# Optimization experiments

Hardware: AMD Instinct MI355X
Metric: run time of the kernel (lower is better)

Reference implementation:

```python
import jax, jax.numpy as jnp
import numpy as np

_SAMPLING_EPS = 1e-5


def setup_inputs() -> dict:
    key = jax.random.key(0)
    k1, k2, k3, k4, k5 = jax.random.split(key, 5)
    B, V = 128, 128000
    logits = jax.random.normal(k1, (B, V), dtype=jnp.float32)
    temperature = jax.random.uniform(k2, (B,), dtype=jnp.float32)  # some rows < eps -> greedy
    top_k = jax.random.randint(k3, (B,), 1, 64, dtype=jnp.int32)   # in [1, 63]
    top_p = jax.random.uniform(k4, (B,), dtype=jnp.float32, minval=0.05, maxval=1.0)
    noise_u = jax.random.uniform(k5, (B, V), dtype=jnp.float32, minval=1e-10, maxval=1.0)
    return {"logits": logits, "temperature": temperature, "top_k": top_k,
            "top_p": top_p, "noise_u": noise_u, "max_num_logprobs": 5}


def _apply_top_k_top_p(logits, k, p):
    # Faithful to vLLM: ascending sort, top-k threshold mask, top-p cumsum mask, scatter back.
    B, V = logits.shape
    order = jnp.argsort(logits, axis=-1)                       # ascending, [B, V]
    logits_sort = jnp.take_along_axis(logits, order, axis=-1)
    neg_inf = jnp.float32(-jnp.inf)
    # top-k: pivot value at position V - k; everything strictly below it -> -inf
    pivot_idx = (V - k.astype(jnp.int32))[:, None]             # [B, 1]
    pivot = jnp.take_along_axis(logits_sort, pivot_idx, axis=-1)
    logits_sort = jnp.where(logits_sort < pivot, neg_inf, logits_sort)
    # top-p: softmax over sorted logits, cumsum, drop prefix with mass <= 1 - p (keep last)
    probs_sort = jax.nn.softmax(logits_sort, axis=-1)
    probs_sum = jnp.cumsum(probs_sort, axis=-1)
    top_p_mask = probs_sum <= (1.0 - p)[:, None]
    top_p_mask = top_p_mask.at[:, -1].set(False)
    logits_sort = jnp.where(top_p_mask, neg_inf, logits_sort)
    # scatter back to original vocab order
    rows = jnp.arange(B)[:, None]
    return jnp.zeros_like(logits).at[rows, order].set(logits_sort)


def reference(logits, temperature, top_k, top_p, noise_u, max_num_logprobs):
    # temperature scaling (temp < eps means greedy; divide by 1.0 instead)
    temp = jnp.where(temperature < _SAMPLING_EPS, 1.0, temperature)
    logits = logits.astype(jnp.float32) / temp[:, None]
    # top-k / top-p filtering
    logits = _apply_top_k_top_p(logits, top_k, top_p)
    # probabilities and sampling
    probs = jax.nn.softmax(logits, axis=-1)
    greedy = jnp.argmax(probs, axis=-1)
    q = -jnp.log(noise_u)                                      # Exp(1) noise (q.exponential_())
    random = jnp.argmax(probs / q, axis=-1)
    sampled = jnp.where(temperature < _SAMPLING_EPS, greedy, random).astype(jnp.int32)
    # top-k logprobs
    logprobs = jax.nn.log_softmax(logits, axis=-1)
    topk_logprobs, topk_indices = jax.lax.top_k(logprobs, max_num_logprobs)
    return sampled, topk_indices.astype(jnp.int32), topk_logprobs
```

## Files before the change

### kernel.cpp

```cpp
#include <hip/hip_runtime.h>
#include <math.h>
#include <stdint.h>

#define BT     256
#define NCHUNK 8
#define CAP    4096
#define TOPC   64
#define TILE   (BT * 8)
#define NC     (NCHUNK * TOPC)

__device__ __forceinline__ unsigned f2ord(float f) {
    unsigned u = __float_as_uint(f);
    return u ^ ((u & 0x80000000u) ? 0xFFFFFFFFu : 0x80000000u);
}
__device__ __forceinline__ float ord2f(unsigned k) {
    unsigned u = (k & 0x80000000u) ? (k ^ 0x80000000u) : (k ^ 0xFFFFFFFFu);
    return __uint_as_float(u);
}

__device__ unsigned radix_select_compact(unsigned* s_key, int* s_idx,
                                         unsigned* s_ckey, int* s_cidx,
                                         unsigned* s_hist, unsigned* p_cnt2,
                                         unsigned n, int tid)
{
    unsigned prefix = 0u;
    int remaining = TOPC;
    for (int shift = 28; shift >= 0; shift -= 4) {
        if (tid < 16) s_hist[tid] = 0u;
        __syncthreads();
        for (unsigned i = (unsigned)tid; i < n; i += BT) {
            unsigned k = s_key[i];
            bool ing = (shift == 28) || ((k >> (shift + 4)) == (prefix >> (shift + 4)));
            if (ing) atomicAdd(&s_hist[(k >> shift) & 15u], 1u);
        }
        __syncthreads();
        int cum = 0; int b = 0;
        for (int bb = 15; bb >= 0; --bb) {
            cum += (int)s_hist[bb];
            if (cum >= remaining) { b = bb; break; }
        }
        remaining -= (cum - (int)s_hist[b]);
        prefix |= ((unsigned)b) << shift;
        __syncthreads();
    }
    if (tid == 0) *p_cnt2 = 0u;
    __syncthreads();
    for (unsigned i = (unsigned)tid; i < n; i += BT) {
        unsigned k = s_key[i];
        if (k > prefix) {
            unsigned pos = atomicAdd(p_cnt2, 1u);
            s_ckey[pos] = k; s_cidx[pos] = s_idx[i];
        }
    }
    __syncthreads();
    for (unsigned i = (unsigned)tid; i < n; i += BT) {
        unsigned k = s_key[i];
        if (k == prefix) {
            unsigned pos = atomicAdd(p_cnt2, 1u);
            if (pos < TOPC) { s_ckey[pos] = k; s_cidx[pos] = s_idx[i]; }
        }
    }
    __syncthreads();
    return prefix;
}

__global__ __launch_bounds__(BT) void phase1_topk_chunks(
    const float* __restrict__ logits, uint2* __restrict__ cand,
    int V, int chunk_len)
{
    __shared__ unsigned s_key[CAP];
    __shared__ int      s_idx[CAP];
    __shared__ unsigned s_ckey[TOPC];
    __shared__ int      s_cidx[TOPC];
    __shared__ unsigned s_hist[16];
    __shared__ unsigned s_cnt, s_cnt2, s_thr;

    const int row   = blockIdx.y;
    const int chunk = blockIdx.x;
    const int tid   = threadIdx.x;
    const int lane  = tid & 63;
    const int c0    = chunk * chunk_len;
    int c1 = c0 + chunk_len; if (c1 > V) c1 = V;
    const float* rowp = logits + (size_t)row * (size_t)V;

    if (tid == 0) { s_cnt = 0u; s_thr = 0u; }
    __syncthreads();

    for (int t0 = c0; t0 < c1; t0 += TILE) {
        unsigned cnt = s_cnt;
        if (cnt + TILE > CAP) {
            unsigned vstar = radix_select_compact(s_key, s_idx, s_ckey, s_cidx,
                                                  s_hist, &s_cnt2, cnt, tid);
            if (tid < TOPC) { s_key[tid] = s_ckey[tid]; s_idx[tid] = s_cidx[tid]; }
            if (tid == 0)   { s_cnt = TOPC; s_thr = vstar; }
            __syncthreads();
        }
        unsigned thr = s_thr;
        int base = t0 + tid * 8;
        unsigned k[8];
        if (base < c1) {
            float4 a = *(const float4*)(rowp + base);
            float4 b = *(const float4*)(rowp + base + 4);
            k[0] = f2ord(a.x); k[1] = f2ord(a.y); k[2] = f2ord(a.z); k[3] = f2ord(a.w);
            k[4] = f2ord(b.x); k[5] = f2ord(b.y); k[6] = f2ord(b.z); k[7] = f2ord(b.w);
        } else {
            #pragma unroll
            for (int j = 0; j < 8; ++j) k[j] = 0u;
        }
        #pragma unroll
        for (int j = 0; j < 8; ++j) {
            bool pass = (k[j] > thr);
            unsigned long long mask = __ballot(pass);
            if (mask) {
                int leader = __ffsll((unsigned long long)mask) - 1;
                unsigned b0 = 0u;
                if (lane == leader)
                    b0 = atomicAdd(&s_cnt, (unsigned)__popcll(mask));
                b0 = __shfl(b0, leader);
                if (pass) {
                    unsigned pos = b0 + (unsigned)__popcll(mask & ((1ull << lane) - 1ull));
                    s_key[pos] = k[j];
                    s_idx[pos] = base + j;
                }
            }
        }
        __syncthreads();
    }

    unsigned cnt = s_cnt;
    radix_select_compact(s_key, s_idx, s_ckey, s_cidx, s_hist, &s_cnt2, cnt, tid);
    if (tid < TOPC) {
        cand[((size_t)row * NCHUNK + chunk) * TOPC + tid] =
            make_uint2(s_ckey[tid], (unsigned)s_cidx[tid]);
    }
}

__global__ __launch_bounds__(BT) void phase2_sample(
    const uint2* __restrict__ cand,
    const float* __restrict__ temperature,
    const int*   __restrict__ top_k,
    const float* __restrict__ top_p,
    const float* __restrict__ noise_u,
    float* __restrict__ out,
    int B, int V, int M)
{
    __shared__ unsigned key[NC];
    __shared__ int      idx[NC];
    __shared__ float    sval[TOPC], se[TOPC], sq[TOPC];
    __shared__ int      sidx[TOPC];

    const int r   = blockIdx.x;
    const int tid = threadIdx.x;

    for (int i = tid; i < NC; i += BT) {
        uint2 c = cand[(size_t)r * NC + i];
        key[i] = c.x; idx[i] = (int)c.y;
    }
    __syncthreads();

    for (int kk = 2; kk <= NC; kk <<= 1) {
        for (int j = kk >> 1; j > 0; j >>= 1) {
            int t  = tid;
            int i0 = ((t & ~(j - 1)) << 1) | (t & (j - 1));
            int i1 = i0 | j;
            bool up = ((i0 & kk) == 0);
            unsigned ka = key[i0], kb = key[i1];
            int ia = idx[i0], ib = idx[i1];
            bool gt = (ka > kb) || (ka == kb && ia < ib);
            if (gt == up) { key[i0] = kb; key[i1] = ka; idx[i0] = ib; idx[i1] = ia; }
            __syncthreads();
        }
    }

    float temp_orig = temperature[r];
    float temp = (temp_orig < 1e-5f) ? 1.0f : temp_orig;

    if (tid < TOPC) {
        unsigned k = key[NC - 1 - tid];
        int id = idx[NC - 1 - tid];
        sval[tid] = ord2f(k) / temp;
        sidx[tid] = id;
        float u = noise_u[(size_t)r * (size_t)V + id];
        sq[tid] = -logf(u);
    }
    __syncthreads();
    if (tid < TOPC) se[tid] = expf(sval[tid] - sval[0]);
    __syncthreads();

    if (tid == 0) {
        int k = top_k[r];
        if (k < 1) k = 1; if (k > TOPC) k = TOPC;
        float p = top_p[r];

        float pivot = sval[k - 1];
        int m = k;
        while (m < TOPC && sval[m] >= pivot) ++m;

        float sum = 0.f;
        for (int i = 0; i < m; ++i) sum += se[i];

        float thr1 = 1.0f - p;
        float S = 0.f;
        int f = 1;
        for (int i = m - 1; i >= 1; --i) {
            S += se[i] / sum;
            if (S > thr1) { f = i + 1; break; }
        }

        float sum2 = 0.f;
        for (int i = 0; i < f; ++i) sum2 += se[i];

        int greedy = sidx[0];
        float best = -1.f; int bidx = 0x7fffffff;
        for (int i = 0; i < f; ++i) {
            float ratio = (se[i] / sum2) / sq[i];
            if (ratio > best || (ratio == best && sidx[i] < bidx)) {
                best = ratio; bidx = sidx[i];
            }
        }
        int sampled = (temp_orig < 1e-5f) ? greedy : bidx;

        float lse = logf(sum2);
        out[r] = (float)sampled;
        float* oidx = out + B + (size_t)r * M;
        float* olp  = out + B + (size_t)B * M + (size_t)r * M;
        int produced = 0;
        for (int i = 0; i < f && produced < M; ++i, ++produced) {
            oidx[produced] = (float)sidx[i];
            olp[produced]  = (sval[i] - sval[0]) - lse;
        }
        int v = 0;
        while (produced < M) {
            bool used = false;
            for (int i = 0; i < f; ++i) if (sidx[i] == v) { used = true; break; }
            if (!used) { oidx[produced] = (float)v; olp[produced] = -3.0e38f; ++produced; }
            ++v;
        }
    }
}

extern "C" void kernel_launch(void* const* d_in, const int* in_sizes, int n_in,
                              void* d_out, int out_size, void* d_ws, size_t ws_size,
                              hipStream_t stream)
{
    const float* logits      = (const float*)d_in[0];
    const float* temperature = (const float*)d_in[1];
    const int*   top_k       = (const int*)d_in[2];
    const float* top_p       = (const float*)d_in[3];
    const float* noise_u     = (const float*)d_in[4];

    const int B = in_sizes[1];
    const int V = in_sizes[0] / B;
    const int M = (out_size / B - 1) / 2;

    uint2* cand = (uint2*)d_ws;

    int chunk_len = (((V + NCHUNK - 1) / NCHUNK) + 7) & ~7;

    dim3 g1(NCHUNK, B);
    phase1_topk_chunks<<<g1, BT, 0, stream>>>(logits, cand, V, chunk_len);
    phase2_sample<<<B, BT, 0, stream>>>(cand, temperature, top_k, top_p, noise_u,
                                        (float*)d_out, B, V, M);
}
```

Measured before the change: 188.2 us.

## Replace per-chunk streaming radix select with global histogram threshold then gather

Swaps the per-chunk streaming top-64 selection, which repeatedly compacted shared-memory buffers, for a two-pass scheme. The first pass builds a 2048-bin histogram of the high key bits per row, a small kernel finds the bin threshold that covers the top 64, and a second pass gathers every element at or above that threshold into a global candidate list. Phase 2 then runs one radix select over those candidates and sorts only 64 entries instead of sorting 512. This reads the logits twice and adds a memset plus two launches. If many values share the threshold bin, candidates past the 2048 capacity are dropped, which could give wrong top-k results on some input distributions.

```diff
diff --git a/kernel.cpp b/kernel.cpp
--- a/kernel.cpp
+++ b/kernel.cpp
@@ -2,12 +2,12 @@
 #include <math.h>
 #include <stdint.h>
 
-#define BT     256
+#define BT    256
 #define NCHUNK 8
-#define CAP    4096
-#define TOPC   64
-#define TILE   (BT * 8)
-#define NC     (NCHUNK * TOPC)
+#define BINS  2048
+#define SHIFT 21
+#define TOPC  64
+#define CAP2  2048
 
 __device__ __forceinline__ unsigned f2ord(float f) {
     unsigned u = __float_as_uint(f);
@@ -18,10 +18,128 @@
     return __uint_as_float(u);
 }
 
-__device__ unsigned radix_select_compact(unsigned* s_key, int* s_idx,
-                                         unsigned* s_ckey, int* s_cidx,
-                                         unsigned* s_hist, unsigned* p_cnt2,
-                                         unsigned n, int tid)
+__global__ __launch_bounds__(BT) void passA_hist(
+    const float* __restrict__ logits, unsigned* __restrict__ hist,
+    int V, int chunk_len)
+{
+    __shared__ unsigned h[BINS];
+    const int row = blockIdx.y, chunk = blockIdx.x, tid = threadIdx.x;
+    const int c0 = chunk * chunk_len;
+    int c1 = c0 + chunk_len; if (c1 > V) c1 = V;
+    const float* rowp = logits + (size_t)row * (size_t)V;
+
+    for (int i = tid; i < BINS; i += BT) h[i] = 0u;
+    __syncthreads();
+
+    for (int base = c0 + tid * 16; base < c1; base += BT * 16) {
+        if (base + 16 <= c1) {
+            float4 a = *(const float4*)(rowp + base);
+            float4 b = *(const float4*)(rowp + base + 4);
+            float4 c = *(const float4*)(rowp + base + 8);
+            float4 d = *(const float4*)(rowp + base + 12);
+            const float v[16] = {a.x,a.y,a.z,a.w, b.x,b.y,b.z,b.w,
+                                 c.x,c.y,c.z,c.w, d.x,d.y,d.z,d.w};
+            #pragma unroll
+            for (int j = 0; j < 16; ++j)
+                atomicAdd(&h[f2ord(v[j]) >> SHIFT], 1u);
+        } else {
+            for (int j = 0; base + j < c1; ++j)
+                atomicAdd(&h[f2ord(rowp[base + j]) >> SHIFT], 1u);
+        }
+    }
+    __syncthreads();
+    for (int i = tid; i < BINS; i += BT) {
+        unsigned v = h[i];
+        if (v) atomicAdd(&hist[(size_t)row * BINS + i], v);
+    }
+}
+
+__global__ __launch_bounds__(BT) void passT_threshold(
+    const unsigned* __restrict__ hist, unsigned* __restrict__ thr, int B)
+{
+    __shared__ unsigned h[BINS];
+    __shared__ unsigned seg[BT];
+    const int r = blockIdx.x, tid = threadIdx.x;
+
+    for (int i = tid; i < BINS; i += BT) h[i] = hist[(size_t)r * BINS + i];
+    __syncthreads();
+
+    unsigned s = 0;
+    #pragma unroll
+    for (int j = 0; j < BINS / BT; ++j) s += h[tid * (BINS / BT) + j];
+    seg[tid] = s;
+    __syncthreads();
+    for (int off = 1; off < BT; off <<= 1) {
+        unsigned v = (tid + off < BT) ? seg[tid + off] : 0u;
+        __syncthreads();
+        seg[tid] += v;
+        __syncthreads();
+    }
+    unsigned sfx_next = (tid + 1 < BT) ? seg[tid + 1] : 0u;
+    if (seg[tid] >= TOPC && sfx_next < TOPC) {
+        unsigned running = sfx_next;
+        int T = tid * (BINS / BT);
+        for (int b = tid * (BINS / BT) + (BINS / BT) - 1; b >= tid * (BINS / BT); --b) {
+            running += h[b];
+            if (running >= TOPC) { T = b; break; }
+        }
+        thr[r] = ((unsigned)T) << SHIFT;
+    }
+}
+
+__global__ __launch_bounds__(BT) void passB_gather(
+    const float* __restrict__ logits, const unsigned* __restrict__ thr,
+    unsigned* __restrict__ cnt, uint2* __restrict__ cand,
+    int V, int chunk_len)
+{
+    const int row = blockIdx.y, chunk = blockIdx.x, tid = threadIdx.x;
+    const int lane = tid & 63;
+    const int c0 = chunk * chunk_len;
+    int c1 = c0 + chunk_len; if (c1 > V) c1 = V;
+    const float* rowp = logits + (size_t)row * (size_t)V;
+    const unsigned t = thr[row];
+
+    for (int base = c0 + tid * 16; base < c1; base += BT * 16) {
+        unsigned k[16];
+        int nval;
+        if (base + 16 <= c1) {
+            float4 a = *(const float4*)(rowp + base);
+            float4 b = *(const float4*)(rowp + base + 4);
+            float4 c = *(const float4*)(rowp + base + 8);
+            float4 d = *(const float4*)(rowp + base + 12);
+            const float v[16] = {a.x,a.y,a.z,a.w, b.x,b.y,b.z,b.w,
+                                 c.x,c.y,c.z,c.w, d.x,d.y,d.z,d.w};
+            #pragma unroll
+            for (int j = 0; j < 16; ++j) k[j] = f2ord(v[j]);
+            nval = 16;
+        } else {
+            nval = c1 - base;
+            for (int j = 0; j < nval; ++j) k[j] = f2ord(rowp[base + j]);
+        }
+        #pragma unroll
+        for (int j = 0; j < 16; ++j) {
+            bool pass = (j < nval) && (k[j] >= t);
+            unsigned long long mask = __ballot(pass);
+            if (mask) {
+                int leader = __ffsll((unsigned long long)mask) - 1;
+                unsigned b0 = 0u;
+                if (lane == leader)
+                    b0 = atomicAdd(&cnt[row], (unsigned)__popcll(mask));
+                b0 = __shfl(b0, leader);
+                if (pass) {
+                    unsigned pos = b0 + (unsigned)__popcll(mask & ((1ull << lane) - 1ull));
+                    if (pos < CAP2)
+                        cand[(size_t)row * CAP2 + pos] = make_uint2(k[j], (unsigned)(base + j));
+                }
+            }
+        }
+    }
+}
+
+__device__ void radix_select_compact(unsigned* s_key, int* s_idx,
+                                     unsigned* s_ckey, int* s_cidx,
+                                     unsigned* s_hist, unsigned* p_cnt2,
+                                     unsigned n, int tid)
 {
     unsigned prefix = 0u;
     int remaining = TOPC;
@@ -61,82 +179,10 @@
         }
     }
     __syncthreads();
-    return prefix;
-}
-
-__global__ __launch_bounds__(BT) void phase1_topk_chunks(
-    const float* __restrict__ logits, uint2* __restrict__ cand,
-    int V, int chunk_len)
-{
-    __shared__ unsigned s_key[CAP];
-    __shared__ int      s_idx[CAP];
-    __shared__ unsigned s_ckey[TOPC];
-    __shared__ int      s_cidx[TOPC];
-    __shared__ unsigned s_hist[16];
-    __shared__ unsigned s_cnt, s_cnt2, s_thr;
-
-    const int row   = blockIdx.y;
-    const int chunk = blockIdx.x;
-    const int tid   = threadIdx.x;
-    const int lane  = tid & 63;
-    const int c0    = chunk * chunk_len;
-    int c1 = c0 + chunk_len; if (c1 > V) c1 = V;
-    const float* rowp = logits + (size_t)row * (size_t)V;
-
-    if (tid == 0) { s_cnt = 0u; s_thr = 0u; }
-    __syncthreads();
-
-    for (int t0 = c0; t0 < c1; t0 += TILE) {
-        unsigned cnt = s_cnt;
-        if (cnt + TILE > CAP) {
-            unsigned vstar = radix_select_compact(s_key, s_idx, s_ckey, s_cidx,
-                                                  s_hist, &s_cnt2, cnt, tid);
-            if (tid < TOPC) { s_key[tid] = s_ckey[tid]; s_idx[tid] = s_cidx[tid]; }
-            if (tid == 0)   { s_cnt = TOPC; s_thr = vstar; }
-            __syncthreads();
-        }
-        unsigned thr = s_thr;
-        int base = t0 + tid * 8;
-        unsigned k[8];
-        if (base < c1) {
-            float4 a = *(const float4*)(rowp + base);
-            float4 b = *(const float4*)(rowp + base + 4);
-            k[0] = f2ord(a.x); k[1] = f2ord(a.y); k[2] = f2ord(a.z); k[3] = f2ord(a.w);
-            k[4] = f2ord(b.x); k[5] = f2ord(b.y); k[6] = f2ord(b.z); k[7] = f2ord(b.w);
-        } else {
-            #pragma unroll
-            for (int j = 0; j < 8; ++j) k[j] = 0u;
-        }
-        #pragma unroll
-        for (int j = 0; j < 8; ++j) {
-            bool pass = (k[j] > thr);
-            unsigned long long mask = __ballot(pass);
-            if (mask) {
-                int leader = __ffsll((unsigned long long)mask) - 1;
-                unsigned b0 = 0u;
-                if (lane == leader)
-                    b0 = atomicAdd(&s_cnt, (unsigned)__popcll(mask));
-                b0 = __shfl(b0, leader);
-                if (pass) {
-                    unsigned pos = b0 + (unsigned)__popcll(mask & ((1ull << lane) - 1ull));
-                    s_key[pos] = k[j];
-                    s_idx[pos] = base + j;
-                }
-            }
-        }
-        __syncthreads();
-    }
-
-    unsigned cnt = s_cnt;
-    radix_select_compact(s_key, s_idx, s_ckey, s_cidx, s_hist, &s_cnt2, cnt, tid);
-    if (tid < TOPC) {
-        cand[((size_t)row * NCHUNK + chunk) * TOPC + tid] =
-            make_uint2(s_ckey[tid], (unsigned)s_cidx[tid]);
-    }
 }
 
 __global__ __launch_bounds__(BT) void phase2_sample(
-    const uint2* __restrict__ cand,
+    const unsigned* __restrict__ cnt, const uint2* __restrict__ cand,
     const float* __restrict__ temperature,
     const int*   __restrict__ top_k,
     const float* __restrict__ top_p,
@@ -144,30 +190,38 @@
     float* __restrict__ out,
     int B, int V, int M)
 {
-    __shared__ unsigned key[NC];
-    __shared__ int      idx[NC];
+    __shared__ unsigned key[CAP2];
+    __shared__ int      idx[CAP2];
+    __shared__ unsigned ckey[TOPC];
+    __shared__ int      cidx[TOPC];
+    __shared__ unsigned hist16[16];
+    __shared__ unsigned cnt2;
     __shared__ float    sval[TOPC], se[TOPC], sq[TOPC];
     __shared__ int      sidx[TOPC];
 
-    const int r   = blockIdx.x;
-    const int tid = threadIdx.x;
-
-    for (int i = tid; i < NC; i += BT) {
-        uint2 c = cand[(size_t)r * NC + i];
+    const int r = blockIdx.x, tid = threadIdx.x;
+
+    unsigned n = cnt[r];
+    if (n > CAP2) n = CAP2;
+    for (unsigned i = (unsigned)tid; i < n; i += BT) {
+        uint2 c = cand[(size_t)r * CAP2 + i];
         key[i] = c.x; idx[i] = (int)c.y;
     }
     __syncthreads();
 
-    for (int kk = 2; kk <= NC; kk <<= 1) {
+    radix_select_compact(key, idx, ckey, cidx, hist16, &cnt2, n, tid);
+
+    for (int kk = 2; kk <= TOPC; kk <<= 1) {
         for (int j = kk >> 1; j > 0; j >>= 1) {
-            int t  = tid;
-            int i0 = ((t & ~(j - 1)) << 1) | (t & (j - 1));
-            int i1 = i0 | j;
-            bool up = ((i0 & kk) == 0);
-            unsigned ka = key[i0], kb = key[i1];
-            int ia = idx[i0], ib = idx[i1];
-            bool gt = (ka > kb) || (ka == kb && ia < ib);
-            if (gt == up) { key[i0] = kb; key[i1] = ka; idx[i0] = ib; idx[i1] = ia; }
+            if (tid < TOPC / 2) {
+                int i0 = ((tid & ~(j - 1)) << 1) | (tid & (j - 1));
+                int i1 = i0 | j;
+                bool up = ((i0 & kk) == 0);
+                unsigned ka = ckey[i0], kb = ckey[i1];
+                int ia = cidx[i0], ib = cidx[i1];
+                bool gt = (ka > kb) || (ka == kb && ia < ib);
+                if (gt == up) { ckey[i0] = kb; ckey[i1] = ka; cidx[i0] = ib; cidx[i1] = ia; }
+            }
             __syncthreads();
         }
     }
@@ -176,8 +230,8 @@
     float temp = (temp_orig < 1e-5f) ? 1.0f : temp_orig;
 
     if (tid < TOPC) {
-        unsigned k = key[NC - 1 - tid];
-        int id = idx[NC - 1 - tid];
+        unsigned k = ckey[TOPC - 1 - tid];
+        int id = cidx[TOPC - 1 - tid];
         sval[tid] = ord2f(k) / temp;
         sidx[tid] = id;
         float u = noise_u[(size_t)r * (size_t)V + id];
@@ -253,12 +307,20 @@
     const int V = in_sizes[0] / B;
     const int M = (out_size / B - 1) / 2;
 
-    uint2* cand = (uint2*)d_ws;
-
-    int chunk_len = (((V + NCHUNK - 1) / NCHUNK) + 7) & ~7;
-
-    dim3 g1(NCHUNK, B);
-    phase1_topk_chunks<<<g1, BT, 0, stream>>>(logits, cand, V, chunk_len);
-    phase2_sample<<<B, BT, 0, stream>>>(cand, temperature, top_k, top_p, noise_u,
-                                        (float*)d_out, B, V, M);
-}
+    char* w = (char*)d_ws;
+    unsigned* cnt  = (unsigned*)w;
+    unsigned* hist = (unsigned*)(w + 1024);
+    unsigned* thr  = (unsigned*)(w + 1024 + (size_t)B * BINS * 4);
+    uint2*    cand = (uint2*)   (w + 1024 + (size_t)B * BINS * 4 + 1024);
+
+    hipMemsetAsync(d_ws, 0, 1024 + (size_t)B * BINS * 4, stream);
+
+    int chunk_len = (((V + NCHUNK - 1) / NCHUNK) + 15) & ~15;
+
+    dim3 g(NCHUNK, B);
+    passA_hist     <<<g, BT, 0, stream>>>(logits, hist, V, chunk_len);
+    passT_threshold<<<B, BT, 0, stream>>>(hist, thr, B);
+    passB_gather   <<<g, BT, 0, stream>>>(logits, thr, cnt, cand, V, chunk_len);
+    phase2_sample  <<<B, BT, 0, stream>>>(cnt, cand, temperature, top_k, top_p,
+                                          noise_u, (float*)d_out, B, V, M);
+}
```

After: 218.0 us. 15.8% more time.

## Presample threshold per chunk, quadruple chunk count, radix-select candidates before sorting

Applied to the files above, without the earlier changes.

Phase 1 now uses 32 chunks per row instead of 8 for more parallelism. Each chunk first samples 1024 values and radix-selects their 64th largest as an initial threshold, so far fewer elements are pushed into shared memory. The ballot-based wave compaction is replaced by per-element LDS atomics, and a scalar tail loop handles V not divisible by 4. Phase 2 radix-selects the top 64 from the 2048 candidates before running a 64-element bitonic sort, instead of sorting all candidates.

```diff
diff --git a/kernel.cpp b/kernel.cpp
--- a/kernel.cpp
+++ b/kernel.cpp
@@ -3,10 +3,11 @@
 #include <stdint.h>
 
 #define BT     256
-#define NCHUNK 8
-#define CAP    4096
+#define NCHUNK 32
 #define TOPC   64
-#define TILE   (BT * 8)
+#define CAP    3072
+#define CAPA   (CAP + 8)
+#define TILE4  (BT * 2)
 #define NC     (NCHUNK * TOPC)
 
 __device__ __forceinline__ unsigned f2ord(float f) {
@@ -64,75 +65,86 @@
     return prefix;
 }
 
-__global__ __launch_bounds__(BT) void phase1_topk_chunks(
+__global__ __launch_bounds__(BT) void fused_select(
     const float* __restrict__ logits, uint2* __restrict__ cand,
-    int V, int chunk_len)
-{
-    __shared__ unsigned s_key[CAP];
-    __shared__ int      s_idx[CAP];
+    int V, int chunk4)
+{
+    __shared__ unsigned s_key[CAPA];
+    __shared__ int      s_idx[CAPA];
     __shared__ unsigned s_ckey[TOPC];
     __shared__ int      s_cidx[TOPC];
     __shared__ unsigned s_hist[16];
-    __shared__ unsigned s_cnt, s_cnt2, s_thr;
-
-    const int row   = blockIdx.y;
-    const int chunk = blockIdx.x;
-    const int tid   = threadIdx.x;
-    const int lane  = tid & 63;
-    const int c0    = chunk * chunk_len;
-    int c1 = c0 + chunk_len; if (c1 > V) c1 = V;
-    const float* rowp = logits + (size_t)row * (size_t)V;
-
-    if (tid == 0) { s_cnt = 0u; s_thr = 0u; }
-    __syncthreads();
-
-    for (int t0 = c0; t0 < c1; t0 += TILE) {
+    __shared__ unsigned s_cnt, s_cnt2;
+    __shared__ float    s_tf;
+
+    const int row = blockIdx.y, chunk = blockIdx.x, tid = threadIdx.x;
+    const int V4 = V >> 2;
+    const int c0 = chunk * chunk4;
+    int c1 = c0 + chunk4; if (c1 > V4) c1 = V4;
+    const float4* rp = (const float4*)(logits + (size_t)row * (size_t)V);
+
+    int stride = (c1 - c0) / BT; if (stride < 1) stride = 1;
+    int si = c0 + tid * stride; if (si >= c1) si = c1 - 1;
+    {
+        float4 sv = rp[si];
+        s_key[tid * 4 + 0] = f2ord(sv.x); s_idx[tid * 4 + 0] = si * 4 + 0;
+        s_key[tid * 4 + 1] = f2ord(sv.y); s_idx[tid * 4 + 1] = si * 4 + 1;
+        s_key[tid * 4 + 2] = f2ord(sv.z); s_idx[tid * 4 + 2] = si * 4 + 2;
+        s_key[tid * 4 + 3] = f2ord(sv.w); s_idx[tid * 4 + 3] = si * 4 + 3;
+    }
+    __syncthreads();
+    unsigned vs = radix_select_compact(s_key, s_idx, s_ckey, s_cidx,
+                                       s_hist, &s_cnt2, BT * 4, tid);
+    if (tid == 0) { s_cnt = 0u; s_tf = ord2f(vs); }
+    __syncthreads();
+    float tf = s_tf;
+
+    for (int base = c0; base < c1; base += TILE4) {
         unsigned cnt = s_cnt;
-        if (cnt + TILE > CAP) {
+        if (cnt + TILE4 * 4 > CAP) {
             unsigned vstar = radix_select_compact(s_key, s_idx, s_ckey, s_cidx,
                                                   s_hist, &s_cnt2, cnt, tid);
             if (tid < TOPC) { s_key[tid] = s_ckey[tid]; s_idx[tid] = s_cidx[tid]; }
-            if (tid == 0)   { s_cnt = TOPC; s_thr = vstar; }
+            if (tid == 0)   { s_cnt = TOPC; s_tf = ord2f(vstar); }
             __syncthreads();
-        }
-        unsigned thr = s_thr;
-        int base = t0 + tid * 8;
-        unsigned k[8];
-        if (base < c1) {
-            float4 a = *(const float4*)(rowp + base);
-            float4 b = *(const float4*)(rowp + base + 4);
-            k[0] = f2ord(a.x); k[1] = f2ord(a.y); k[2] = f2ord(a.z); k[3] = f2ord(a.w);
-            k[4] = f2ord(b.x); k[5] = f2ord(b.y); k[6] = f2ord(b.z); k[7] = f2ord(b.w);
-        } else {
-            #pragma unroll
-            for (int j = 0; j < 8; ++j) k[j] = 0u;
-        }
-        #pragma unroll
-        for (int j = 0; j < 8; ++j) {
-            bool pass = (k[j] > thr);
-            unsigned long long mask = __ballot(pass);
-            if (mask) {
-                int leader = __ffsll((unsigned long long)mask) - 1;
-                unsigned b0 = 0u;
-                if (lane == leader)
-                    b0 = atomicAdd(&s_cnt, (unsigned)__popcll(mask));
-                b0 = __shfl(b0, leader);
-                if (pass) {
-                    unsigned pos = b0 + (unsigned)__popcll(mask & ((1ull << lane) - 1ull));
-                    s_key[pos] = k[j];
-                    s_idx[pos] = base + j;
-                }
-            }
-        }
-        __syncthreads();
-    }
-
-    unsigned cnt = s_cnt;
-    radix_select_compact(s_key, s_idx, s_ckey, s_cidx, s_hist, &s_cnt2, cnt, tid);
-    if (tid < TOPC) {
+            tf = s_tf;
+        }
+        int i0 = base + tid;
+        int i1 = base + BT + tid;
+        int j0 = i0 < c1 ? i0 : c1 - 1;
+        int j1 = i1 < c1 ? i1 : c1 - 1;
+        float4 a = rp[j0];
+        float4 b = rp[j1];
+        if (i0 < c1) {
+            int g = i0 * 4;
+            if (a.x >= tf) { unsigned p = atomicAdd(&s_cnt, 1u); s_key[p] = f2ord(a.x); s_idx[p] = g + 0; }
+            if (a.y >= tf) { unsigned p = atomicAdd(&s_cnt, 1u); s_key[p] = f2ord(a.y); s_idx[p] = g + 1; }
+            if (a.z >= tf) { unsigned p = atomicAdd(&s_cnt, 1u); s_key[p] = f2ord(a.z); s_idx[p] = g + 2; }
+            if (a.w >= tf) { unsigned p = atomicAdd(&s_cnt, 1u); s_key[p] = f2ord(a.w); s_idx[p] = g + 3; }
+        }
+        if (i1 < c1) {
+            int g = i1 * 4;
+            if (b.x >= tf) { unsigned p = atomicAdd(&s_cnt, 1u); s_key[p] = f2ord(b.x); s_idx[p] = g + 0; }
+            if (b.y >= tf) { unsigned p = atomicAdd(&s_cnt, 1u); s_key[p] = f2ord(b.y); s_idx[p] = g + 1; }
+            if (b.z >= tf) { unsigned p = atomicAdd(&s_cnt, 1u); s_key[p] = f2ord(b.z); s_idx[p] = g + 2; }
+            if (b.w >= tf) { unsigned p = atomicAdd(&s_cnt, 1u); s_key[p] = f2ord(b.w); s_idx[p] = g + 3; }
+        }
+        __syncthreads();
+    }
+
+    if (chunk == NCHUNK - 1 && tid == 0) {
+        const float* rowp = logits + (size_t)row * (size_t)V;
+        for (int j = V4 * 4; j < V; ++j) {
+            float v = rowp[j];
+            if (v >= s_tf) { unsigned p = atomicAdd(&s_cnt, 1u); s_key[p] = f2ord(v); s_idx[p] = j; }
+        }
+    }
+    __syncthreads();
+
+    radix_select_compact(s_key, s_idx, s_ckey, s_cidx, s_hist, &s_cnt2, s_cnt, tid);
+    if (tid < TOPC)
         cand[((size_t)row * NCHUNK + chunk) * TOPC + tid] =
             make_uint2(s_ckey[tid], (unsigned)s_cidx[tid]);
-    }
 }
 
 __global__ __launch_bounds__(BT) void phase2_sample(
@@ -146,11 +158,14 @@
 {
     __shared__ unsigned key[NC];
     __shared__ int      idx[NC];
+    __shared__ unsigned ckey[TOPC];
+    __shared__ int      cidx[TOPC];
+    __shared__ unsigned hist16[16];
+    __shared__ unsigned cnt2;
     __shared__ float    sval[TOPC], se[TOPC], sq[TOPC];
     __shared__ int      sidx[TOPC];
 
-    const int r   = blockIdx.x;
-    const int tid = threadIdx.x;
+    const int r = blockIdx.x, tid = threadIdx.x;
 
     for (int i = tid; i < NC; i += BT) {
         uint2 c = cand[(size_t)r * NC + i];
@@ -158,16 +173,19 @@
     }
     __syncthreads();
 
-    for (int kk = 2; kk <= NC; kk <<= 1) {
+    radix_select_compact(key, idx, ckey, cidx, hist16, &cnt2, NC, tid);
+
+    for (int kk = 2; kk <= TOPC; kk <<= 1) {
         for (int j = kk >> 1; j > 0; j >>= 1) {
-            int t  = tid;
-            int i0 = ((t & ~(j - 1)) << 1) | (t & (j - 1));
-            int i1 = i0 | j;
-            bool up = ((i0 & kk) == 0);
-            unsigned ka = key[i0], kb = key[i1];
-            int ia = idx[i0], ib = idx[i1];
-            bool gt = (ka > kb) || (ka == kb && ia < ib);
-            if (gt == up) { key[i0] = kb; key[i1] = ka; idx[i0] = ib; idx[i1] = ia; }
+            if (tid < TOPC / 2) {
+                int i0 = ((tid & ~(j - 1)) << 1) | (tid & (j - 1));
+                int i1 = i0 | j;
+                bool up = ((i0 & kk) == 0);
+                unsigned ka = ckey[i0], kb = ckey[i1];
+                int ia = cidx[i0], ib = cidx[i1];
+                bool gt = (ka > kb) || (ka == kb && ia < ib);
+                if (gt == up) { ckey[i0] = kb; ckey[i1] = ka; cidx[i0] = ib; cidx[i1] = ia; }
+            }
             __syncthreads();
         }
     }
@@ -176,8 +194,8 @@
     float temp = (temp_orig < 1e-5f) ? 1.0f : temp_orig;
 
     if (tid < TOPC) {
-        unsigned k = key[NC - 1 - tid];
-        int id = idx[NC - 1 - tid];
+        unsigned k = ckey[TOPC - 1 - tid];
+        int id = cidx[TOPC - 1 - tid];
         sval[tid] = ord2f(k) / temp;
         sidx[tid] = id;
         float u = noise_u[(size_t)r * (size_t)V + id];
@@ -255,10 +273,11 @@
 
     uint2* cand = (uint2*)d_ws;
 
-    int chunk_len = (((V + NCHUNK - 1) / NCHUNK) + 7) & ~7;
-
-    dim3 g1(NCHUNK, B);
-    phase1_topk_chunks<<<g1, BT, 0, stream>>>(logits, cand, V, chunk_len);
-    phase2_sample<<<B, BT, 0, stream>>>(cand, temperature, top_k, top_p, noise_u,
-                                        (float*)d_out, B, V, M);
-}
+    const int V4 = V >> 2;
+    const int chunk4 = (V4 + NCHUNK - 1) / NCHUNK;
+
+    dim3 g(NCHUNK, B);
+    fused_select <<<g, BT, 0, stream>>>(logits, cand, V, chunk4);
+    phase2_sample<<<B, BT, 0, stream>>>(cand, temperature, top_k, top_p,
+                                        noise_u, (float*)d_out, B, V, M);
+}
```

Measured after the change: 214.4 us. 1.14x slower.
